# Kernel tuning notes

Measured on AMD Instinct MI355X. Metric: run time of the kernel, lower is better.

## Reference

```python
import jax, jax.numpy as jnp
import numpy as np

NODE_DIM, HIDDEN, PROJ = 5, 128, 256
NUM_MP = 3
BOX = 1.0


def _knn_edges(positions, k, box_length=BOX):
    """Periodic kNN graph. positions: (B,N,3) -> (src, dst) global flat indices, E = B*N*k."""
    B, N, _ = positions.shape

    def per_batch(pos):  # (N,3)
        delta = jnp.abs(pos[:, None, :] - pos[None, :, :])          # (N,N,3)
        delta = jnp.where(delta > 0.5 * box_length, box_length - delta, delta)
        dist = jnp.sqrt(jnp.sum(delta * delta, axis=-1) + 1e-12)    # (N,N)
        _, idx = jax.lax.top_k(-dist, k + 1)                        # k+1 smallest
        return idx[:, 1:]                                           # drop self -> (N,k)

    nbrs = jax.vmap(per_batch)(positions)                           # (B,N,k)
    offset = (jnp.arange(B) * N)[:, None, None]
    src = jnp.broadcast_to(jnp.arange(N)[None, :, None], (B, N, k)) + offset
    dst = nbrs + offset
    return src.reshape(-1), dst.reshape(-1)


def setup_inputs() -> dict:
    key = jax.random.key(0)
    ks = jax.random.split(key, 16)
    B, N = 8, 2048
    s = 0.05
    inp = {
        "x": jax.random.normal(ks[0], (B, N, NODE_DIM), jnp.float32),
        "positions": jax.random.uniform(ks[1], (B, N, 3), jnp.float32),
        "k": 16,
        # encoder: Linear(5,128)+ReLU, Linear(128,128)+ReLU
        "enc_w0": jax.random.normal(ks[2], (NODE_DIM, HIDDEN), jnp.float32) * s,
        "enc_b0": jnp.zeros((HIDDEN,), jnp.float32),
        "enc_w1": jax.random.normal(ks[3], (HIDDEN, HIDDEN), jnp.float32) * s,
        "enc_b1": jnp.zeros((HIDDEN,), jnp.float32),
        # message nets: Linear(2H,H)+ReLU per round
        "msg_w": jax.random.normal(ks[4], (NUM_MP, 2 * HIDDEN, HIDDEN), jnp.float32) * s,
        "msg_b": jnp.zeros((NUM_MP, HIDDEN), jnp.float32),
        # update nets: Linear(2H,H)+ReLU per round
        "upd_w": jax.random.normal(ks[5], (NUM_MP, 2 * HIDDEN, HIDDEN), jnp.float32) * s,
        "upd_b": jnp.zeros((NUM_MP, HIDDEN), jnp.float32),
        # projection head: Linear(H,H)+ReLU, Linear(H,proj)
        "proj_w0": jax.random.normal(ks[6], (HIDDEN, HIDDEN), jnp.float32) * s,
        "proj_b0": jnp.zeros((HIDDEN,), jnp.float32),
        "proj_w1": jax.random.normal(ks[7], (HIDDEN, PROJ), jnp.float32) * s,
        "proj_b1": jnp.zeros((PROJ,), jnp.float32),
    }
    return inp


def reference(x, positions, k, enc_w0, enc_b0, enc_w1, enc_b1,
              msg_w, msg_b, upd_w, upd_b, proj_w0, proj_b0, proj_w1, proj_b1):
    B, N, _ = x.shape
    BN = B * N
    relu = jax.nn.relu

    # encoder over flattened nodes
    h = relu(x.reshape(BN, -1) @ enc_w0 + enc_b0)
    h = relu(h @ enc_w1 + enc_b1)

    src, dst = _knn_edges(positions, k)
    E = src.shape[0]
    deg = jax.ops.segment_sum(jnp.ones((E,), h.dtype), dst, num_segments=BN)
    inv_deg = 1.0 / jnp.clip(deg, 1.0)

    for i in range(NUM_MP):
        # per-edge message: concat(sender, receiver) -> Linear+ReLU
        msg = relu(jnp.concatenate([h[src], h[dst]], axis=-1) @ msg_w[i] + msg_b[i])
        # mean aggregation at destination nodes
        agg = jax.ops.segment_sum(msg, dst, num_segments=BN) * inv_deg[:, None]
        # residual update
        h = h + relu(jnp.concatenate([h, agg], axis=-1) @ upd_w[i] + upd_b[i])

    z = relu(h @ proj_w0 + proj_b0) @ proj_w1 + proj_b1
    return z.reshape(B, N, PROJ), h.reshape(B, N, HIDDEN)
```

## Files before the change

### kernel.cpp

```cpp
#include <hip/hip_runtime.h>
#include <stdint.h>
#include <math.h>

#define NN 2048
#define BB 8
#define BN (BB*NN)
#define KK 16
#define EE (BN*KK)
#define HID 128
#define PROJ_D 256
#define QPB 16

typedef unsigned long long u64;
typedef unsigned short ushort_t;
typedef __attribute__((ext_vector_type(8))) short short8;
typedef __attribute__((ext_vector_type(4))) float f32x4;

__device__ __forceinline__ u64 wave_min_u64(u64 v) {
  #pragma unroll
  for (int off = 32; off > 0; off >>= 1) {
    u64 o = __shfl_xor(v, off);
    v = o < v ? o : v;
  }
  return v;
}

__global__ __launch_bounds__(1024) void knn_kernel(const float* __restrict__ pos,
                                                   int* __restrict__ nbr,
                                                   int* __restrict__ cnt) {
  __shared__ float4 Ps[NN];
  __shared__ unsigned Hist[QPB * 256];
  const int b  = blockIdx.x >> 7;
  const int qb = blockIdx.x & 127;
  const int wave = threadIdx.x >> 6;
  const int lane = threadIdx.x & 63;
  const int i = qb * QPB + wave;
  const float* P = pos + (size_t)b * NN * 3;

  for (int t = threadIdx.x; t < NN; t += 1024)
    Ps[t] = make_float4(P[t*3], P[t*3+1], P[t*3+2], 0.f);
  __syncthreads();

  const float4 pi = Ps[i];
  const float xi = pi.x, yi = pi.y, zi = pi.z;
  unsigned* H = &Hist[wave * 256];

  float d[32];
  #pragma unroll
  for (int t = 0; t < 32; t++) {
    int j = t * 64 + lane;
    float4 pj = Ps[j];
    float ax = fabsf(xi - pj.x), ay = fabsf(yi - pj.y), az = fabsf(zi - pj.z);
    float dx = fminf(ax, 1.0f - ax);
    float dy = fminf(ay, 1.0f - ay);
    float dz = fminf(az, 1.0f - az);
    float s = __fadd_rn(__fadd_rn(__fadd_rn(__fmul_rn(dx,dx), __fmul_rn(dy,dy)),
                                  __fmul_rn(dz,dz)), 1e-12f);
    d[t] = __fsqrt_rn(s);
  }

  float scale = 1024.0f;
  int bstar = 0; unsigned C = 0;
  for (;;) {
    *(uint4*)&H[lane * 4] = make_uint4(0u, 0u, 0u, 0u);
    #pragma unroll
    for (int t = 0; t < 32; t++) {
      int bin = (int)(d[t] * scale);
      if (bin < 256) atomicAdd(&H[bin], 1u);
    }
    uint4 cv = *(const uint4*)&H[lane * 4];
    unsigned s4 = cv.x + cv.y + cv.z + cv.w;
    unsigned incl = s4;
    #pragma unroll
    for (int off = 1; off < 64; off <<= 1) {
      unsigned v = __shfl_up(incl, off);
      if (lane >= off) incl += v;
    }
    unsigned total = __shfl(incl, 63);
    if (total >= 17u) {
      unsigned base = incl - s4;
      bool has = (incl >= 17u) && (base < 17u);
      u64 hmask = __ballot(has);
      int srcl = __ffsll((unsigned long long)hmask) - 1;
      int bl = 0; unsigned Cl = 0;
      if (has) {
        if (base + cv.x >= 17u)                    { bl = lane*4 + 0; Cl = base; }
        else if (base + cv.x + cv.y >= 17u)        { bl = lane*4 + 1; Cl = base + cv.x; }
        else if (base + cv.x + cv.y + cv.z >= 17u) { bl = lane*4 + 2; Cl = base + cv.x + cv.y; }
        else                                       { bl = lane*4 + 3; Cl = base + cv.x + cv.y + cv.z; }
      }
      bstar = __shfl(bl, srcl);
      C     = __shfl(Cl, srcl);
      break;
    }
    scale *= 0.25f;
  }
  const int m = 17 - (int)C;

  u64 lst[6];
  #pragma unroll
  for (int t = 0; t < 6; t++) lst[t] = ~0ull;
  #pragma unroll
  for (int t = 0; t < 32; t++) {
    int bin = (int)(d[t] * scale);
    u64 key = ((u64)__float_as_uint(d[t]) << 11) | (unsigned)(t * 64 + lane);
    u64 cand = (bin == bstar) ? key : ~0ull;
    if (cand < lst[5]) {
      lst[5] = cand;
      #pragma unroll
      for (int u = 5; u > 0; u--) {
        u64 a = lst[u-1], c2 = lst[u];
        lst[u-1] = a < c2 ? a : c2;
        lst[u]   = a < c2 ? c2 : a;
      }
    }
  }

  u64 kstar = 0;
  #pragma unroll 1
  for (int r = 0; r < m; r++) {
    u64 h0 = lst[0];
    u64 gm = wave_min_u64(h0);
    kstar = gm;
    bool win = (h0 == gm);
    #pragma unroll
    for (int u = 0; u < 5; u++) lst[u] = win ? lst[u+1] : lst[u];
    lst[5] = win ? ~0ull : lst[5];
  }

  int* outp = nbr + ((size_t)b * NN + i) * KK;
  int total = 0;
  #pragma unroll
  for (int t = 0; t < 32; t++) {
    int j = t * 64 + lane;
    u64 key = ((u64)__float_as_uint(d[t]) << 11) | (unsigned)j;
    bool pred = (key <= kstar) && (j != i);
    u64 msk = __ballot(pred);
    if (pred) {
      int ofs = total + __popcll(msk & ((1ull << lane) - 1ull));
      outp[ofs] = b * NN + j;
      atomicAdd(&cnt[b * NN + j], 1);
    }
    total += __popcll(msk);
  }
}

__global__ __launch_bounds__(256) void scan_kernel(const int* __restrict__ cnt,
                                                   int* __restrict__ row_ptr) {
  __shared__ int ps[256];
  int t = threadIdx.x;
  const int4* cv = (const int4*)(cnt + t * 64);
  int4 c[16];
  int s = 0;
  #pragma unroll
  for (int i = 0; i < 16; i++) {
    c[i] = cv[i];
    s += c[i].x + c[i].y + c[i].z + c[i].w;
  }
  ps[t] = s;
  __syncthreads();
  for (int off = 1; off < 256; off <<= 1) {
    int v = 0;
    if (t >= off) v = ps[t - off];
    __syncthreads();
    ps[t] += v;
    __syncthreads();
  }
  int run = t ? ps[t - 1] : 0;
  int4* rp = (int4*)(row_ptr + t * 64);
  #pragma unroll
  for (int i = 0; i < 16; i++) {
    int4 o;
    o.x = run; run += c[i].x;
    o.y = run; run += c[i].y;
    o.z = run; run += c[i].z;
    o.w = run; run += c[i].w;
    rp[i] = o;
  }
  if (t == 255) row_ptr[BN] = run;
}

__global__ __launch_bounds__(256) void fill_kernel(const int* __restrict__ nbr,
                                                   const int* __restrict__ row_ptr,
                                                   int* __restrict__ fill,
                                                   int* __restrict__ col) {
  int e = blockIdx.x * 256 + threadIdx.x;
  int d = nbr[e];
  int srcn = e >> 4;
  int p = row_ptr[d] + atomicAdd(&fill[d], 1);
  col[p] = srcn;
}

__global__ __launch_bounds__(256) void enc0_kernel(const float* __restrict__ x,
                                                   const float* __restrict__ w0,
                                                   const float* __restrict__ b0,
                                                   float* __restrict__ h) {
  int t = blockIdx.x * 256 + threadIdx.x;
  int m = t >> 5;
  int c = (t & 31) * 4;
  float xv[5];
  #pragma unroll
  for (int d = 0; d < 5; d++) xv[d] = x[m * 5 + d];
  float4 acc = *(const float4*)&b0[c];
  #pragma unroll
  for (int d = 0; d < 5; d++) {
    float4 w = *(const float4*)&w0[d * HID + c];
    acc.x += xv[d] * w.x; acc.y += xv[d] * w.y;
    acc.z += xv[d] * w.z; acc.w += xv[d] * w.w;
  }
  acc.x = fmaxf(acc.x, 0.f); acc.y = fmaxf(acc.y, 0.f);
  acc.z = fmaxf(acc.z, 0.f); acc.w = fmaxf(acc.w, 0.f);
  *(float4*)&h[(size_t)m * HID + c] = acc;
}


__device__ __forceinline__ ushort_t bf16_rne(float x) {
  unsigned u = __float_as_uint(x);
  unsigned r = u + 0x7FFFu + ((u >> 16) & 1u);
  return (ushort_t)(r >> 16);
}
__device__ __forceinline__ float bf16_to_f(ushort_t h) {
  return __uint_as_float(((unsigned)h) << 16);
}

__device__ __forceinline__ void cvt8(const float4 f0, const float4 f1,
                                     short8& hi, short8& lo) {
  float f[8] = {f0.x, f0.y, f0.z, f0.w, f1.x, f1.y, f1.z, f1.w};
  #pragma unroll
  for (int e = 0; e < 8; e++) {
    ushort_t h = bf16_rne(f[e]);
    ushort_t l = bf16_rne(f[e] - bf16_to_f(h));
    hi[e] = (short)h;
    lo[e] = (short)l;
  }
}

__global__ __launch_bounds__(256) void prep_w_kernel(
    const float* __restrict__ enc_w1, const float* __restrict__ msg_w,
    const float* __restrict__ upd_w, const float* __restrict__ proj_w0,
    const float* __restrict__ proj_w1, ushort_t* __restrict__ wfrag) {
  int u = blockIdx.x >> 3;
  int c = (blockIdx.x & 7) * 256 + threadIdx.x;
  const float* src;
  int ldW = HID;
  if (u == 0) src = enc_w1;
  else if (u <= 6)  { int i = (u-1)>>1; int hf = (u-1)&1; src = msg_w + ((size_t)i*256 + hf*128) * HID; }
  else if (u <= 12) { int i = (u-7)>>1; int hf = (u-7)&1; src = upd_w + ((size_t)i*256 + hf*128) * HID; }
  else if (u == 13) src = proj_w0;
  else { src = proj_w1 + (u - 14) * 128; ldW = PROJ_D; }

  int ks = c >> 9, ct = (c >> 6) & 7, lane = c & 63;
  int colc = ct * 16 + (lane & 15);
  int k0 = ks * 32 + ((lane >> 4) << 3);
  float f[8];
  #pragma unroll
  for (int e = 0; e < 8; e++) f[e] = src[(size_t)(k0 + e) * ldW + colc];
  short8 hv, lv;
  cvt8(make_float4(f[0],f[1],f[2],f[3]), make_float4(f[4],f[5],f[6],f[7]), hv, lv);
  *(short8*)&wfrag[(size_t)u * 32768 + (size_t)c * 8] = hv;
  *(short8*)&wfrag[(size_t)u * 32768 + 16384 + (size_t)c * 8] = lv;
}

template<int PHASES, int RELU, int HASRES>
__device__ __forceinline__ void gemm_mfma_body(
    const float* __restrict__ A1, const ushort_t* __restrict__ wf1,
    const float* __restrict__ A2, const ushort_t* __restrict__ wf2,
    const float* __restrict__ bias, const float* __restrict__ Res,
    float* __restrict__ out, int ldOut, int n0,
    ushort_t* Ahi, ushort_t* Alo, ushort_t* Bhi, ushort_t* Blo) {
  const int tid = threadIdx.x, lane = tid & 63, wid = tid >> 6;
  const int m0 = blockIdx.x * 64;
  f32x4 zero = {0.f, 0.f, 0.f, 0.f};
  f32x4 acc[8];
  #pragma unroll
  for (int ct = 0; ct < 8; ct++) acc[ct] = zero;

  #pragma unroll 1
  for (int ph = 0; ph < PHASES; ph++) {
    const float* A = ph ? A2 : A1;
    const ushort_t* wf = ph ? wf2 : wf1;
    #pragma unroll
    for (int i = 0; i < 4; i++) {
      int c = tid + i * 256;
      int row = c >> 4, kg = c & 15;
      const float4* ap = (const float4*)(A + (((size_t)m0 + row) << 7) + (kg << 3));
      short8 hv, lv;
      cvt8(ap[0], ap[1], hv, lv);
      int idx = (((row >> 4) * 4 + (kg >> 2)) * 64 + ((row & 15) | ((kg & 3) << 4))) * 8;
      *(short8*)&Ahi[idx] = hv;
      *(short8*)&Alo[idx] = lv;
    }
    #pragma unroll 1
    for (int half = 0; half < 2; half++) {
      const short8* ghi = (const short8*)(wf + half * 8192);
      const short8* glo = (const short8*)(wf + 16384 + half * 8192);
      #pragma unroll
      for (int i = 0; i < 4; i++) {
        ((short8*)Bhi)[tid + i * 256] = ghi[tid + i * 256];
        ((short8*)Blo)[tid + i * 256] = glo[tid + i * 256];
      }
      __syncthreads();
      #pragma unroll
      for (int ks2 = 0; ks2 < 2; ks2++) {
        int ksA = half * 2 + ks2;
        short8 ah = *(const short8*)&Ahi[((wid * 4 + ksA) * 64 + lane) * 8];
        short8 al = *(const short8*)&Alo[((wid * 4 + ksA) * 64 + lane) * 8];
        #pragma unroll
        for (int ct = 0; ct < 8; ct++) {
          short8 bh = *(const short8*)&Bhi[((ks2 * 8 + ct) * 64 + lane) * 8];
          short8 bl = *(const short8*)&Blo[((ks2 * 8 + ct) * 64 + lane) * 8];
          acc[ct] = __builtin_amdgcn_mfma_f32_16x16x32_bf16(ah, bh, acc[ct], 0, 0, 0);
          acc[ct] = __builtin_amdgcn_mfma_f32_16x16x32_bf16(ah, bl, acc[ct], 0, 0, 0);
          acc[ct] = __builtin_amdgcn_mfma_f32_16x16x32_bf16(al, bh, acc[ct], 0, 0, 0);
        }
      }
      __syncthreads();
    }
  }

  const int rbase = m0 + wid * 16 + ((lane >> 4) << 2);
  const int cb = lane & 15;
  #pragma unroll
  for (int ct = 0; ct < 8; ct++) {
    int n = n0 + ct * 16 + cb;
    float bv = bias ? bias[n] : 0.f;
    #pragma unroll
    for (int r = 0; r < 4; r++) {
      float v = acc[ct][r] + bv;
      if (RELU) v = fmaxf(v, 0.f);
      if (HASRES) v += Res[(size_t)(rbase + r) * HID + n];
      out[(size_t)(rbase + r) * ldOut + n] = v;
    }
  }
}

template<int RELU>
__global__ __launch_bounds__(256, 4) void g1_kernel(
    const float* __restrict__ A, const ushort_t* __restrict__ wf,
    const float* __restrict__ bias, float* __restrict__ out) {
  __shared__ ushort_t Ahi[8192], Alo[8192], Bhi[8192], Blo[8192];
  gemm_mfma_body<1, RELU, 0>(A, wf, nullptr, nullptr, bias, nullptr,
                             out, HID, 0, Ahi, Alo, Bhi, Blo);
}

__global__ __launch_bounds__(256, 4) void msg_kernel(
    const float* __restrict__ h, const ushort_t* __restrict__ wfT,
    const ushort_t* __restrict__ wfB, const float* __restrict__ mb,
    float* __restrict__ bufA, float* __restrict__ bufB) {
  __shared__ ushort_t Ahi[8192], Alo[8192], Bhi[8192], Blo[8192];
  int y = blockIdx.y;
  gemm_mfma_body<1, 0, 0>(h, y ? wfB : wfT, nullptr, nullptr,
                          y ? mb : nullptr, nullptr, y ? bufB : bufA,
                          HID, 0, Ahi, Alo, Bhi, Blo);
}

__global__ __launch_bounds__(256, 4) void upd_kernel(
    const float* __restrict__ h, const ushort_t* __restrict__ wfT,
    const float* __restrict__ agg, const ushort_t* __restrict__ wfB,
    const float* __restrict__ ub, float* __restrict__ out) {
  __shared__ ushort_t Ahi[8192], Alo[8192], Bhi[8192], Blo[8192];
  gemm_mfma_body<2, 1, 1>(h, wfT, agg, wfB, ub, h,
                          out, HID, 0, Ahi, Alo, Bhi, Blo);
}

__global__ __launch_bounds__(256, 4) void proj1_kernel(
    const float* __restrict__ A, const ushort_t* __restrict__ wf01,
    const float* __restrict__ pb1, float* __restrict__ z) {
  __shared__ ushort_t Ahi[8192], Alo[8192], Bhi[8192], Blo[8192];
  int y = blockIdx.y;
  gemm_mfma_body<1, 0, 0>(A, wf01 + (size_t)y * 32768, nullptr, nullptr,
                          pb1, nullptr, z, PROJ_D, y * 128,
                          Ahi, Alo, Bhi, Blo);
}

__global__ __launch_bounds__(256) void agg_kernel(const float* __restrict__ Abuf,
                                                  const float* __restrict__ Bbuf,
                                                  const int* __restrict__ row_ptr,
                                                  const int* __restrict__ col,
                                                  float* __restrict__ agg) {
  int j = blockIdx.x * 2 + (threadIdx.x >> 7);
  int c = threadIdx.x & 127;
  float bj = Bbuf[(size_t)j * HID + c];
  int s = row_ptr[j], e = row_ptr[j + 1];
  float acc = 0.f;
  int p = s;
  for (; p + 4 <= e; p += 4) {
    int i0 = col[p], i1 = col[p+1], i2 = col[p+2], i3 = col[p+3];
    float v0 = Abuf[(size_t)i0 * HID + c];
    float v1 = Abuf[(size_t)i1 * HID + c];
    float v2 = Abuf[(size_t)i2 * HID + c];
    float v3 = Abuf[(size_t)i3 * HID + c];
    acc += fmaxf(v0 + bj, 0.f) + fmaxf(v1 + bj, 0.f)
         + fmaxf(v2 + bj, 0.f) + fmaxf(v3 + bj, 0.f);
  }
  for (; p < e; p++) {
    int i = col[p];
    acc += fmaxf(Abuf[(size_t)i * HID + c] + bj, 0.f);
  }
  float deg = (float)(e - s);
  float inv = 1.0f / fmaxf(deg, 1.0f);
  agg[(size_t)j * HID + c] = acc * inv;
}

extern "C" void kernel_launch(void* const* d_in, const int* in_sizes, int n_in,
                              void* d_out, int out_size, void* d_ws, size_t ws_size,
                              hipStream_t stream) {
  (void)in_sizes; (void)n_in; (void)out_size; (void)ws_size;
  const float* x       = (const float*)d_in[0];
  const float* pos     = (const float*)d_in[1];
  const float* enc_w0  = (const float*)d_in[3];
  const float* enc_b0  = (const float*)d_in[4];
  const float* enc_w1  = (const float*)d_in[5];
  const float* enc_b1  = (const float*)d_in[6];
  const float* msg_w   = (const float*)d_in[7];
  const float* msg_b   = (const float*)d_in[8];
  const float* upd_w   = (const float*)d_in[9];
  const float* upd_b   = (const float*)d_in[10];
  const float* proj_w0 = (const float*)d_in[11];
  const float* proj_b0 = (const float*)d_in[12];
  const float* proj_w1 = (const float*)d_in[13];
  const float* proj_b1 = (const float*)d_in[14];

  char* ws = (char*)d_ws;
  size_t off = 0;
  auto alloc = [&](size_t bytes) -> void* {
    void* p = ws + off;
    off += (bytes + 255) & ~(size_t)255;
    return p;
  };
  int*      nbr     = (int*)alloc((size_t)EE * 4);
  int*      cnt     = (int*)alloc((size_t)BN * 4);
  int*      fill    = (int*)alloc((size_t)BN * 4);
  int*      row_ptr = (int*)alloc((size_t)(BN + 1) * 4);
  int*      col     = (int*)alloc((size_t)EE * 4);
  float*    h_a     = (float*)alloc((size_t)BN * HID * 4);
  float*    h_b     = (float*)alloc((size_t)BN * HID * 4);
  float*    bufA    = (float*)alloc((size_t)BN * HID * 4);
  float*    bufB    = (float*)alloc((size_t)BN * HID * 4);
  float*    bufAgg  = (float*)alloc((size_t)BN * HID * 4);
  ushort_t* wfrag   = (ushort_t*)alloc((size_t)16 * 32768 * 2);
  float*    out     = (float*)d_out;
  float*    hOut    = out + (size_t)BN * PROJ_D;

  hipMemsetAsync(cnt, 0, (size_t)BN * 4 * 2, stream);

  prep_w_kernel<<<128, 256, 0, stream>>>(enc_w1, msg_w, upd_w, proj_w0, proj_w1, wfrag);

  knn_kernel<<<BN / QPB, 1024, 0, stream>>>(pos, nbr, cnt);
  scan_kernel<<<1, 256, 0, stream>>>(cnt, row_ptr);
  fill_kernel<<<EE / 256, 256, 0, stream>>>(nbr, row_ptr, fill, col);

  enc0_kernel<<<BN * 32 / 256, 256, 0, stream>>>(x, enc_w0, enc_b0, bufA);
  g1_kernel<1><<<BN / 64, 256, 0, stream>>>(bufA, wfrag + 0 * 32768, enc_b1, h_a);

  float* hc = h_a;
  float* hn = h_b;
  for (int i = 0; i < 3; i++) {
    const ushort_t* wmT = wfrag + (size_t)(1 + 2 * i) * 32768;
    const ushort_t* wmB = wfrag + (size_t)(2 + 2 * i) * 32768;
    msg_kernel<<<dim3(BN / 64, 2), 256, 0, stream>>>(
        hc, wmT, wmB, msg_b + (size_t)i * HID, bufA, bufB);
    agg_kernel<<<BN / 2, 256, 0, stream>>>(bufA, bufB, row_ptr, col, bufAgg);
    const ushort_t* wuT = wfrag + (size_t)(7 + 2 * i) * 32768;
    const ushort_t* wuB = wfrag + (size_t)(8 + 2 * i) * 32768;
    float* target = (i == 2) ? hOut : hn;
    upd_kernel<<<BN / 64, 256, 0, stream>>>(
        hc, wuT, bufAgg, wuB, upd_b + (size_t)i * HID, target);
    hn = hc; hc = target;
  }

  g1_kernel<1><<<BN / 64, 256, 0, stream>>>(hc, wfrag + 13 * 32768, proj_b0, bufA);
  proj1_kernel<<<dim3(BN / 64, 2), 256, 0, stream>>>(
      bufA, wfrag + 14 * 32768, proj_b1, out);
}
```

Measured before the change: 244.0 us.

## Fuse encoder/proj GEMM chains and cache hidden state as pre-split bf16 fragments

After: 273.3 us. +12.0%, slower.

```diff
diff --git a/kernel.cpp b/kernel.cpp
--- a/kernel.cpp
+++ b/kernel.cpp
@@ -191,28 +191,6 @@
   col[p] = srcn;
 }
 
-__global__ __launch_bounds__(256) void enc0_kernel(const float* __restrict__ x,
-                                                   const float* __restrict__ w0,
-                                                   const float* __restrict__ b0,
-                                                   float* __restrict__ h) {
-  int t = blockIdx.x * 256 + threadIdx.x;
-  int m = t >> 5;
-  int c = (t & 31) * 4;
-  float xv[5];
-  #pragma unroll
-  for (int d = 0; d < 5; d++) xv[d] = x[m * 5 + d];
-  float4 acc = *(const float4*)&b0[c];
-  #pragma unroll
-  for (int d = 0; d < 5; d++) {
-    float4 w = *(const float4*)&w0[d * HID + c];
-    acc.x += xv[d] * w.x; acc.y += xv[d] * w.y;
-    acc.z += xv[d] * w.z; acc.w += xv[d] * w.w;
-  }
-  acc.x = fmaxf(acc.x, 0.f); acc.y = fmaxf(acc.y, 0.f);
-  acc.z = fmaxf(acc.z, 0.f); acc.w = fmaxf(acc.w, 0.f);
-  *(float4*)&h[(size_t)m * HID + c] = acc;
-}
-
 
 __device__ __forceinline__ ushort_t bf16_rne(float x) {
   unsigned u = __float_as_uint(x);
@@ -261,116 +239,250 @@
   *(short8*)&wfrag[(size_t)u * 32768 + 16384 + (size_t)c * 8] = lv;
 }
 
-template<int PHASES, int RELU, int HASRES>
-__device__ __forceinline__ void gemm_mfma_body(
-    const float* __restrict__ A1, const ushort_t* __restrict__ wf1,
-    const float* __restrict__ A2, const ushort_t* __restrict__ wf2,
-    const float* __restrict__ bias, const float* __restrict__ Res,
-    float* __restrict__ out, int ldOut, int n0,
-    ushort_t* Ahi, ushort_t* Alo, ushort_t* Bhi, ushort_t* Blo) {
-  const int tid = threadIdx.x, lane = tid & 63, wid = tid >> 6;
-  const int m0 = blockIdx.x * 64;
-  f32x4 zero = {0.f, 0.f, 0.f, 0.f};
-  f32x4 acc[8];
-  #pragma unroll
-  for (int ct = 0; ct < 8; ct++) acc[ct] = zero;
-
+__device__ __forceinline__ void zacc(f32x4 acc[8]) {
+  f32x4 z = {0.f, 0.f, 0.f, 0.f};
+  #pragma unroll
+  for (int ct = 0; ct < 8; ct++) acc[ct] = z;
+}
+
+__device__ __forceinline__ void stage_A_linear(ushort_t* Ahi, ushort_t* Alo,
+                                               const ushort_t* gfrag, int tid) {
+  const short8* gh = (const short8*)gfrag;
+  const short8* gl = (const short8*)(gfrag + 8192);
+  #pragma unroll
+  for (int i = 0; i < 4; i++) {
+    ((short8*)Ahi)[tid + i * 256] = gh[tid + i * 256];
+    ((short8*)Alo)[tid + i * 256] = gl[tid + i * 256];
+  }
+}
+
+__device__ __forceinline__ void stage_A_convert(ushort_t* Ahi, ushort_t* Alo,
+                                                const float* A, int m0, int tid) {
+  #pragma unroll
+  for (int i = 0; i < 4; i++) {
+    int c = tid + i * 256;
+    int row = c >> 4, kg = c & 15;
+    const float4* ap = (const float4*)(A + (((size_t)m0 + row) << 7) + (kg << 3));
+    short8 hv, lv;
+    cvt8(ap[0], ap[1], hv, lv);
+    int idx = (((row >> 4) * 4 + (kg >> 2)) * 64 + ((row & 15) | ((kg & 3) << 4))) * 8;
+    *(short8*)&Ahi[idx] = hv;
+    *(short8*)&Alo[idx] = lv;
+  }
+}
+
+__device__ __forceinline__ void ldsF_to_frags(const float* ldsF,
+                                              ushort_t* Ahi, ushort_t* Alo,
+                                              int tid) {
+  #pragma unroll
+  for (int i = 0; i < 4; i++) {
+    int c = tid + i * 256;
+    int row = c >> 4, kg = c & 15;
+    const float4* ap = (const float4*)&ldsF[row * 128 + kg * 8];
+    short8 hv, lv;
+    cvt8(ap[0], ap[1], hv, lv);
+    int idx = (((row >> 4) * 4 + (kg >> 2)) * 64 + ((row & 15) | ((kg & 3) << 4))) * 8;
+    *(short8*)&Ahi[idx] = hv;
+    *(short8*)&Alo[idx] = lv;
+  }
+}
+
+__device__ __forceinline__ void ldsF_emit(const float* ldsF,
+                                          ushort_t* gfrag, float* gf32,
+                                          float* gf32b, int tid) {
+  #pragma unroll
+  for (int i = 0; i < 4; i++) {
+    int c = tid + i * 256;
+    int row = c >> 4, kg = c & 15;
+    const float4* ap = (const float4*)&ldsF[row * 128 + kg * 8];
+    float4 a0 = ap[0], a1 = ap[1];
+    short8 hv, lv;
+    cvt8(a0, a1, hv, lv);
+    int idx = (((row >> 4) * 4 + (kg >> 2)) * 64 + ((row & 15) | ((kg & 3) << 4))) * 8;
+    *(short8*)&gfrag[idx] = hv;
+    *(short8*)&gfrag[8192 + idx] = lv;
+    if (gf32) {
+      float4* op = (float4*)&gf32[(size_t)row * 128 + kg * 8];
+      op[0] = a0; op[1] = a1;
+    }
+    if (gf32b) {
+      float4* op = (float4*)&gf32b[(size_t)row * 128 + kg * 8];
+      op[0] = a0; op[1] = a1;
+    }
+  }
+}
+
+__device__ __forceinline__ void unit_mfma(f32x4 acc[8], const ushort_t* wf,
+                                          const ushort_t* Ahi, const ushort_t* Alo,
+                                          ushort_t* Bhi, ushort_t* Blo,
+                                          int tid, int lane, int wid) {
   #pragma unroll 1
-  for (int ph = 0; ph < PHASES; ph++) {
-    const float* A = ph ? A2 : A1;
-    const ushort_t* wf = ph ? wf2 : wf1;
+  for (int half = 0; half < 2; half++) {
+    __syncthreads();
+    const short8* ghi = (const short8*)(wf + half * 8192);
+    const short8* glo = (const short8*)(wf + 16384 + half * 8192);
     #pragma unroll
     for (int i = 0; i < 4; i++) {
-      int c = tid + i * 256;
-      int row = c >> 4, kg = c & 15;
-      const float4* ap = (const float4*)(A + (((size_t)m0 + row) << 7) + (kg << 3));
-      short8 hv, lv;
-      cvt8(ap[0], ap[1], hv, lv);
-      int idx = (((row >> 4) * 4 + (kg >> 2)) * 64 + ((row & 15) | ((kg & 3) << 4))) * 8;
-      *(short8*)&Ahi[idx] = hv;
-      *(short8*)&Alo[idx] = lv;
-    }
-    #pragma unroll 1
-    for (int half = 0; half < 2; half++) {
-      const short8* ghi = (const short8*)(wf + half * 8192);
-      const short8* glo = (const short8*)(wf + 16384 + half * 8192);
+      ((short8*)Bhi)[tid + i * 256] = ghi[tid + i * 256];
+      ((short8*)Blo)[tid + i * 256] = glo[tid + i * 256];
+    }
+    __syncthreads();
+    #pragma unroll
+    for (int ks2 = 0; ks2 < 2; ks2++) {
+      int ksA = half * 2 + ks2;
+      short8 ah = *(const short8*)&Ahi[((wid * 4 + ksA) * 64 + lane) * 8];
+      short8 al = *(const short8*)&Alo[((wid * 4 + ksA) * 64 + lane) * 8];
       #pragma unroll
-      for (int i = 0; i < 4; i++) {
-        ((short8*)Bhi)[tid + i * 256] = ghi[tid + i * 256];
-        ((short8*)Blo)[tid + i * 256] = glo[tid + i * 256];
+      for (int ct = 0; ct < 8; ct++) {
+        short8 bh = *(const short8*)&Bhi[((ks2 * 8 + ct) * 64 + lane) * 8];
+        short8 bl = *(const short8*)&Blo[((ks2 * 8 + ct) * 64 + lane) * 8];
+        acc[ct] = __builtin_amdgcn_mfma_f32_16x16x32_bf16(ah, bh, acc[ct], 0, 0, 0);
+        acc[ct] = __builtin_amdgcn_mfma_f32_16x16x32_bf16(ah, bl, acc[ct], 0, 0, 0);
+        acc[ct] = __builtin_amdgcn_mfma_f32_16x16x32_bf16(al, bh, acc[ct], 0, 0, 0);
       }
-      __syncthreads();
-      #pragma unroll
-      for (int ks2 = 0; ks2 < 2; ks2++) {
-        int ksA = half * 2 + ks2;
-        short8 ah = *(const short8*)&Ahi[((wid * 4 + ksA) * 64 + lane) * 8];
-        short8 al = *(const short8*)&Alo[((wid * 4 + ksA) * 64 + lane) * 8];
-        #pragma unroll
-        for (int ct = 0; ct < 8; ct++) {
-          short8 bh = *(const short8*)&Bhi[((ks2 * 8 + ct) * 64 + lane) * 8];
-          short8 bl = *(const short8*)&Blo[((ks2 * 8 + ct) * 64 + lane) * 8];
-          acc[ct] = __builtin_amdgcn_mfma_f32_16x16x32_bf16(ah, bh, acc[ct], 0, 0, 0);
-          acc[ct] = __builtin_amdgcn_mfma_f32_16x16x32_bf16(ah, bl, acc[ct], 0, 0, 0);
-          acc[ct] = __builtin_amdgcn_mfma_f32_16x16x32_bf16(al, bh, acc[ct], 0, 0, 0);
-        }
-      }
-      __syncthreads();
-    }
-  }
-
-  const int rbase = m0 + wid * 16 + ((lane >> 4) << 2);
-  const int cb = lane & 15;
+    }
+  }
+}
+
+__device__ __forceinline__ void epi_store_f32(const f32x4 acc[8], const float* bias,
+                                              float* out, int ldOut, int n0,
+                                              int m0, int lane, int wid) {
+  int rbase = m0 + wid * 16 + ((lane >> 4) << 2);
+  int cb = lane & 15;
   #pragma unroll
   for (int ct = 0; ct < 8; ct++) {
     int n = n0 + ct * 16 + cb;
     float bv = bias ? bias[n] : 0.f;
     #pragma unroll
+    for (int r = 0; r < 4; r++)
+      out[(size_t)(rbase + r) * ldOut + n] = acc[ct][r] + bv;
+  }
+}
+
+__device__ __forceinline__ void epi_to_ldsF(const f32x4 acc[8], const float* bias,
+                                            float* ldsF, int lane, int wid,
+                                            const float* Res, int m0) {
+  int rloc = wid * 16 + ((lane >> 4) << 2);
+  int cb = lane & 15;
+  #pragma unroll
+  for (int ct = 0; ct < 8; ct++) {
+    int n = ct * 16 + cb;
+    float bv = bias ? bias[n] : 0.f;
+    #pragma unroll
     for (int r = 0; r < 4; r++) {
-      float v = acc[ct][r] + bv;
-      if (RELU) v = fmaxf(v, 0.f);
-      if (HASRES) v += Res[(size_t)(rbase + r) * HID + n];
-      out[(size_t)(rbase + r) * ldOut + n] = v;
-    }
-  }
-}
-
-template<int RELU>
-__global__ __launch_bounds__(256, 4) void g1_kernel(
-    const float* __restrict__ A, const ushort_t* __restrict__ wf,
-    const float* __restrict__ bias, float* __restrict__ out) {
-  __shared__ ushort_t Ahi[8192], Alo[8192], Bhi[8192], Blo[8192];
-  gemm_mfma_body<1, RELU, 0>(A, wf, nullptr, nullptr, bias, nullptr,
-                             out, HID, 0, Ahi, Alo, Bhi, Blo);
-}
-
-__global__ __launch_bounds__(256, 4) void msg_kernel(
-    const float* __restrict__ h, const ushort_t* __restrict__ wfT,
+      float v = fmaxf(acc[ct][r] + bv, 0.f);
+      if (Res) v += Res[(size_t)(m0 + rloc + r) * HID + n];
+      ldsF[(rloc + r) * 128 + n] = v;
+    }
+  }
+}
+
+#define LDS_DECL \
+  __shared__ char LDSBUF[65536]; \
+  ushort_t* Ahi = (ushort_t*)LDSBUF; \
+  ushort_t* Alo = (ushort_t*)(LDSBUF + 16384); \
+  ushort_t* Bhi = (ushort_t*)(LDSBUF + 32768); \
+  ushort_t* Blo = (ushort_t*)(LDSBUF + 49152); \
+  float* ldsF = (float*)(LDSBUF + 32768); \
+  const int tid = threadIdx.x, lane = tid & 63, wid = tid >> 6; \
+  const int m0 = blockIdx.x * 64;
+
+__global__ __launch_bounds__(256, 2) void encg1_kernel(
+    const float* __restrict__ x, const float* __restrict__ ew0,
+    const float* __restrict__ eb0, const ushort_t* __restrict__ wf_enc1,
+    const float* __restrict__ eb1, float* __restrict__ hF32,
+    ushort_t* __restrict__ hfrag) {
+  LDS_DECL
+  float* XWs = (float*)LDSBUF;
+  const int tx = tid & 31, ty = tid >> 5;
+
+  if (tid < 80) ((float4*)XWs)[tid] = ((const float4*)(x + (size_t)m0 * 5))[tid];
+  if (tid < 160) ((float4*)(XWs + 320))[tid] = ((const float4*)ew0)[tid];
+  __syncthreads();
+  {
+    float4 bv = *(const float4*)&eb0[tx * 4];
+    #pragma unroll
+    for (int r = 0; r < 8; r++) {
+      int row = ty + r * 8;
+      float4 a = bv;
+      #pragma unroll
+      for (int d = 0; d < 5; d++) {
+        float xv = XWs[row * 5 + d];
+        float4 w = *(const float4*)&XWs[320 + d * 128 + tx * 4];
+        a.x += xv*w.x; a.y += xv*w.y; a.z += xv*w.z; a.w += xv*w.w;
+      }
+      a.x = fmaxf(a.x,0.f); a.y = fmaxf(a.y,0.f);
+      a.z = fmaxf(a.z,0.f); a.w = fmaxf(a.w,0.f);
+      *(float4*)&ldsF[row * 128 + tx * 4] = a;
+    }
+  }
+  __syncthreads();
+  ldsF_to_frags(ldsF, Ahi, Alo, tid);
+  f32x4 acc[8];
+  zacc(acc);
+  unit_mfma(acc, wf_enc1, Ahi, Alo, Bhi, Blo, tid, lane, wid);
+  __syncthreads();
+  epi_to_ldsF(acc, eb1, ldsF, lane, wid, nullptr, m0);
+  __syncthreads();
+  ldsF_emit(ldsF, hfrag + (size_t)blockIdx.x * 16384,
+            hF32 + (size_t)m0 * HID, nullptr, tid);
+}
+
+__global__ __launch_bounds__(256, 2) void msg_kernel(
+    const ushort_t* __restrict__ hfrag, const ushort_t* __restrict__ wfT,
     const ushort_t* __restrict__ wfB, const float* __restrict__ mb,
     float* __restrict__ bufA, float* __restrict__ bufB) {
-  __shared__ ushort_t Ahi[8192], Alo[8192], Bhi[8192], Blo[8192];
-  int y = blockIdx.y;
-  gemm_mfma_body<1, 0, 0>(h, y ? wfB : wfT, nullptr, nullptr,
-                          y ? mb : nullptr, nullptr, y ? bufB : bufA,
-                          HID, 0, Ahi, Alo, Bhi, Blo);
-}
-
-__global__ __launch_bounds__(256, 4) void upd_kernel(
-    const float* __restrict__ h, const ushort_t* __restrict__ wfT,
-    const float* __restrict__ agg, const ushort_t* __restrict__ wfB,
-    const float* __restrict__ ub, float* __restrict__ out) {
-  __shared__ ushort_t Ahi[8192], Alo[8192], Bhi[8192], Blo[8192];
-  gemm_mfma_body<2, 1, 1>(h, wfT, agg, wfB, ub, h,
-                          out, HID, 0, Ahi, Alo, Bhi, Blo);
-}
-
-__global__ __launch_bounds__(256, 4) void proj1_kernel(
-    const float* __restrict__ A, const ushort_t* __restrict__ wf01,
+  LDS_DECL
+  stage_A_linear(Ahi, Alo, hfrag + (size_t)blockIdx.x * 16384, tid);
+  f32x4 acc[8];
+  zacc(acc);
+  unit_mfma(acc, wfT, Ahi, Alo, Bhi, Blo, tid, lane, wid);
+  epi_store_f32(acc, nullptr, bufA, HID, 0, m0, lane, wid);
+  zacc(acc);
+  unit_mfma(acc, wfB, Ahi, Alo, Bhi, Blo, tid, lane, wid);
+  epi_store_f32(acc, mb, bufB, HID, 0, m0, lane, wid);
+}
+
+__global__ __launch_bounds__(256, 2) void upd_kernel(
+    const ushort_t* __restrict__ hfrag_cur, const ushort_t* __restrict__ wuT,
+    const float* __restrict__ aggF, const ushort_t* __restrict__ wuB,
+    const float* __restrict__ ub, float* __restrict__ hF32,
+    ushort_t* __restrict__ hfrag_nxt, float* __restrict__ hOutOpt) {
+  LDS_DECL
+  stage_A_linear(Ahi, Alo, hfrag_cur + (size_t)blockIdx.x * 16384, tid);
+  f32x4 acc[8];
+  zacc(acc);
+  unit_mfma(acc, wuT, Ahi, Alo, Bhi, Blo, tid, lane, wid);
+  __syncthreads();
+  stage_A_convert(Ahi, Alo, aggF, m0, tid);
+  unit_mfma(acc, wuB, Ahi, Alo, Bhi, Blo, tid, lane, wid);
+  __syncthreads();
+  epi_to_ldsF(acc, ub, ldsF, lane, wid, hF32, m0);
+  __syncthreads();
+  ldsF_emit(ldsF, hfrag_nxt + (size_t)blockIdx.x * 16384,
+            hF32 + (size_t)m0 * HID,
+            hOutOpt ? hOutOpt + (size_t)m0 * HID : nullptr, tid);
+}
+
+__global__ __launch_bounds__(256, 2) void proj_kernel(
+    const ushort_t* __restrict__ hfrag, const ushort_t* __restrict__ wf0,
+    const float* __restrict__ pb0, const ushort_t* __restrict__ wf1,
     const float* __restrict__ pb1, float* __restrict__ z) {
-  __shared__ ushort_t Ahi[8192], Alo[8192], Bhi[8192], Blo[8192];
-  int y = blockIdx.y;
-  gemm_mfma_body<1, 0, 0>(A, wf01 + (size_t)y * 32768, nullptr, nullptr,
-                          pb1, nullptr, z, PROJ_D, y * 128,
-                          Ahi, Alo, Bhi, Blo);
+  LDS_DECL
+  stage_A_linear(Ahi, Alo, hfrag + (size_t)blockIdx.x * 16384, tid);
+  f32x4 acc[8];
+  zacc(acc);
+  unit_mfma(acc, wf0, Ahi, Alo, Bhi, Blo, tid, lane, wid);
+  __syncthreads();
+  epi_to_ldsF(acc, pb0, ldsF, lane, wid, nullptr, m0);
+  __syncthreads();
+  ldsF_to_frags(ldsF, Ahi, Alo, tid);
+  #pragma unroll 1
+  for (int y = 0; y < 2; y++) {
+    zacc(acc);
+    unit_mfma(acc, wf1 + (size_t)y * 32768, Ahi, Alo, Bhi, Blo, tid, lane, wid);
+    epi_store_f32(acc, pb1, z, PROJ_D, y * 128, m0, lane, wid);
+  }
 }
 
 __global__ __launch_bounds__(256) void agg_kernel(const float* __restrict__ Abuf,
@@ -428,48 +540,47 @@
     off += (bytes + 255) & ~(size_t)255;
     return p;
   };
-  int*      nbr     = (int*)alloc((size_t)EE * 4);
-  int*      cnt     = (int*)alloc((size_t)BN * 4);
-  int*      fill    = (int*)alloc((size_t)BN * 4);
-  int*      row_ptr = (int*)alloc((size_t)(BN + 1) * 4);
-  int*      col     = (int*)alloc((size_t)EE * 4);
-  float*    h_a     = (float*)alloc((size_t)BN * HID * 4);
-  float*    h_b     = (float*)alloc((size_t)BN * HID * 4);
-  float*    bufA    = (float*)alloc((size_t)BN * HID * 4);
-  float*    bufB    = (float*)alloc((size_t)BN * HID * 4);
-  float*    bufAgg  = (float*)alloc((size_t)BN * HID * 4);
-  ushort_t* wfrag   = (ushort_t*)alloc((size_t)16 * 32768 * 2);
-  float*    out     = (float*)d_out;
-  float*    hOut    = out + (size_t)BN * PROJ_D;
+  int*      nbr      = (int*)alloc((size_t)EE * 4);
+  int*      cnt      = (int*)alloc((size_t)BN * 4);
+  int*      fill     = (int*)alloc((size_t)BN * 4);
+  int*      row_ptr  = (int*)alloc((size_t)(BN + 1) * 4);
+  int*      col      = (int*)alloc((size_t)EE * 4);
+  float*    h        = (float*)alloc((size_t)BN * HID * 4);
+  float*    bufA     = (float*)alloc((size_t)BN * HID * 4);
+  float*    bufB     = (float*)alloc((size_t)BN * HID * 4);
+  float*    bufAgg   = (float*)alloc((size_t)BN * HID * 4);
+  ushort_t* wfrag    = (ushort_t*)alloc((size_t)16 * 32768 * 2);
+  ushort_t* hfrag_a  = (ushort_t*)alloc((size_t)256 * 16384 * 2);
+  ushort_t* hfrag_b  = (ushort_t*)alloc((size_t)256 * 16384 * 2);
+  float*    out      = (float*)d_out;
+  float*    hOut     = out + (size_t)BN * PROJ_D;
 
   hipMemsetAsync(cnt, 0, (size_t)BN * 4 * 2, stream);
 
   prep_w_kernel<<<128, 256, 0, stream>>>(enc_w1, msg_w, upd_w, proj_w0, proj_w1, wfrag);
-
   knn_kernel<<<BN / QPB, 1024, 0, stream>>>(pos, nbr, cnt);
   scan_kernel<<<1, 256, 0, stream>>>(cnt, row_ptr);
   fill_kernel<<<EE / 256, 256, 0, stream>>>(nbr, row_ptr, fill, col);
 
-  enc0_kernel<<<BN * 32 / 256, 256, 0, stream>>>(x, enc_w0, enc_b0, bufA);
-  g1_kernel<1><<<BN / 64, 256, 0, stream>>>(bufA, wfrag + 0 * 32768, enc_b1, h_a);
-
-  float* hc = h_a;
-  float* hn = h_b;
+  encg1_kernel<<<BN / 64, 256, 0, stream>>>(x, enc_w0, enc_b0, wfrag,
+                                            enc_b1, h, hfrag_a);
+
+  ushort_t* fcur = hfrag_a;
+  ushort_t* fnxt = hfrag_b;
   for (int i = 0; i < 3; i++) {
-    const ushort_t* wmT = wfrag + (size_t)(1 + 2 * i) * 32768;
-    const ushort_t* wmB = wfrag + (size_t)(2 + 2 * i) * 32768;
-    msg_kernel<<<dim3(BN / 64, 2), 256, 0, stream>>>(
-        hc, wmT, wmB, msg_b + (size_t)i * HID, bufA, bufB);
+    msg_kernel<<<BN / 64, 256, 0, stream>>>(
+        fcur, wfrag + (size_t)(1 + 2 * i) * 32768,
+        wfrag + (size_t)(2 + 2 * i) * 32768, msg_b + (size_t)i * HID,
+        bufA, bufB);
     agg_kernel<<<BN / 2, 256, 0, stream>>>(bufA, bufB, row_ptr, col, bufAgg);
-    const ushort_t* wuT = wfrag + (size_t)(7 + 2 * i) * 32768;
-    const ushort_t* wuB = wfrag + (size_t)(8 + 2 * i) * 32768;
-    float* target = (i == 2) ? hOut : hn;
     upd_kernel<<<BN / 64, 256, 0, stream>>>(
-        hc, wuT, bufAgg, wuB, upd_b + (size_t)i * HID, target);
-    hn = hc; hc = target;
-  }
-
-  g1_kernel<1><<<BN / 64, 256, 0, stream>>>(hc, wfrag + 13 * 32768, proj_b0, bufA);
-  proj1_kernel<<<dim3(BN / 64, 2), 256, 0, stream>>>(
-      bufA, wfrag + 14 * 32768, proj_b1, out);
-}
+        fcur, wfrag + (size_t)(7 + 2 * i) * 32768, bufAgg,
+        wfrag + (size_t)(8 + 2 * i) * 32768, upd_b + (size_t)i * HID,
+        h, fnxt, (i == 2) ? hOut : nullptr);
+    ushort_t* t = fcur; fcur = fnxt; fnxt = t;
+  }
+
+  proj_kernel<<<BN / 64, 256, 0, stream>>>(
+      fcur, wfrag + (size_t)13 * 32768, proj_b0,
+      wfrag + (size_t)14 * 32768, proj_b1, out);
+}
```
